# Kernel tuning notes

Hardware: AMD Instinct MI355X
Metric: run time of the kernel (lower is better)

Reference implementation:

```python
import jax, jax.numpy as jnp
import numpy as np
from jax import lax

B, CIN, H, W = 2, 512, 64, 64
NCLS = 5
CI = CIN // 4      # inter_channels = 128
CQ = CI // 8       # PAM query/key channels = 16
EPS = 1e-5


def setup_inputs() -> dict:
    key = jax.random.key(0)
    it = iter(jax.random.split(key, 48))

    def nrm(shape, s=0.05):
        return jax.random.normal(next(it), shape, jnp.float32) * s

    def bn(c):
        w = jax.random.uniform(next(it), (c,), jnp.float32, 0.5, 1.5)
        b = nrm((c,))
        m = nrm((c,))
        v = jax.random.uniform(next(it), (c,), jnp.float32, 0.5, 1.5)
        return w, b, m, v

    inp = {}
    inp['x'] = jax.random.normal(next(it), (B, CIN, H, W), jnp.float32)
    inp['bn_a_w'], inp['bn_a_b'], inp['bn_a_m'], inp['bn_a_v'] = bn(CIN)
    inp['conv_a_w'] = nrm((CI, CIN, 3, 3))
    inp['bn_c_w'], inp['bn_c_b'], inp['bn_c_m'], inp['bn_c_v'] = bn(CIN)
    inp['conv_c_w'] = nrm((CI, CIN, 3, 3))
    inp['pam_q_w'] = nrm((CQ, CI)); inp['pam_q_b'] = nrm((CQ,))
    inp['pam_k_w'] = nrm((CQ, CI)); inp['pam_k_b'] = nrm((CQ,))
    inp['pam_v_w'] = nrm((CI, CI)); inp['pam_v_b'] = nrm((CI,))
    inp['pam_gamma'] = nrm((1,), 0.5)
    inp['cam_gamma'] = nrm((1,), 0.5)
    inp['bn_a1_w'], inp['bn_a1_b'], inp['bn_a1_m'], inp['bn_a1_v'] = bn(CI)
    inp['conv_a1_w'] = nrm((CIN, CI)); inp['conv_a1_b'] = nrm((CIN,))
    inp['bn_c1_w'], inp['bn_c1_b'], inp['bn_c1_m'], inp['bn_c1_v'] = bn(CI)
    inp['conv_c1_w'] = nrm((CIN, CI)); inp['conv_c1_b'] = nrm((CIN,))
    inp['out_a_w'] = nrm((NCLS, CIN)); inp['out_a_b'] = nrm((NCLS,))
    inp['out_c_w'] = nrm((NCLS, CIN)); inp['out_c_b'] = nrm((NCLS,))
    inp['out_f_w'] = nrm((NCLS, CIN)); inp['out_f_b'] = nrm((NCLS,))
    return inp


def _bn_relu(x, w, b, m, v):
    # eval-mode BatchNorm2d followed by ReLU
    scale = (w / jnp.sqrt(v + EPS))[None, :, None, None]
    shift = (b - m * w / jnp.sqrt(v + EPS))[None, :, None, None]
    return jax.nn.relu(x * scale + shift)


def _conv3(x, w):
    return lax.conv_general_dilated(x, w, (1, 1), 'SAME',
                                    dimension_numbers=('NCHW', 'OIHW', 'NCHW'))


def _conv1(x, w, b):
    # 1x1 conv as channel matmul
    return jnp.einsum('oi,bihw->bohw', w, x) + b[None, :, None, None]


def _pam(x, wq, bq, wk, bk, wv, bv, gamma):
    Bc, C, Hh, Ww = x.shape
    N = Hh * Ww
    q = _conv1(x, wq, bq).reshape(Bc, -1, N)   # [B,CQ,N]
    k = _conv1(x, wk, bk).reshape(Bc, -1, N)   # [B,CQ,N]
    v = _conv1(x, wv, bv).reshape(Bc, C, N)    # [B,C,N]
    energy = jnp.einsum('bcn,bcm->bnm', q, k)  # [B,N,N]
    attn = jax.nn.softmax(energy, axis=-1)
    out = jnp.einsum('bcm,bnm->bcn', v, attn).reshape(Bc, C, Hh, Ww)
    return gamma * out + x


def _cam(x, gamma):
    Bc, C, Hh, Ww = x.shape
    N = Hh * Ww
    f = x.reshape(Bc, C, N)
    energy = jnp.einsum('bcn,bdn->bcd', f, f)                    # [B,C,C]
    energy_new = jnp.max(energy, -1, keepdims=True) - energy
    attn = jax.nn.softmax(energy_new, axis=-1)
    out = jnp.einsum('bcd,bdn->bcn', attn, f).reshape(Bc, C, Hh, Ww)
    return gamma * out + x


def reference(x, bn_a_w, bn_a_b, bn_a_m, bn_a_v, conv_a_w,
              bn_c_w, bn_c_b, bn_c_m, bn_c_v, conv_c_w,
              pam_q_w, pam_q_b, pam_k_w, pam_k_b, pam_v_w, pam_v_b,
              pam_gamma, cam_gamma,
              bn_a1_w, bn_a1_b, bn_a1_m, bn_a1_v, conv_a1_w, conv_a1_b,
              bn_c1_w, bn_c1_b, bn_c1_m, bn_c1_v, conv_c1_w, conv_c1_b,
              out_a_w, out_a_b, out_c_w, out_c_b, out_f_w, out_f_b):
    # position-attention branch
    sa = _conv3(_bn_relu(x, bn_a_w, bn_a_b, bn_a_m, bn_a_v), conv_a_w)
    sa = _pam(sa, pam_q_w, pam_q_b, pam_k_w, pam_k_b, pam_v_w, pam_v_b, pam_gamma)
    sa = _conv1(_bn_relu(sa, bn_a1_w, bn_a1_b, bn_a1_m, bn_a1_v), conv_a1_w, conv_a1_b)
    # channel-attention branch
    sc = _conv3(_bn_relu(x, bn_c_w, bn_c_b, bn_c_m, bn_c_v), conv_c_w)
    sc = _cam(sc, cam_gamma)
    sc = _conv1(_bn_relu(sc, bn_c1_w, bn_c1_b, bn_c1_m, bn_c1_v), conv_c1_w, conv_c1_b)
    feat_fusion = sa + sc
    # dropout is identity at eval time
    sa_out = _conv1(sa, out_a_w, out_a_b)
    sc_out = _conv1(sc, out_c_w, out_c_b)
    sasc_out = _conv1(feat_fusion, out_f_w, out_f_b)
    return (feat_fusion, sasc_out, sa_out, sc_out)
```

## Files before the change

kernel.cpp:

```cpp
#include <hip/hip_runtime.h>

using u16 = unsigned short;
using short8 = __attribute__((ext_vector_type(8))) short;
using f32x4 = __attribute__((ext_vector_type(4))) float;

struct alignas(8) U16x4 { u16 x, y, z, w; };

__device__ __forceinline__ float bf2f(u16 u) {
  return __uint_as_float(((unsigned int)u) << 16);
}
__device__ __forceinline__ u16 f2bf(float f) {
  unsigned int u = __float_as_uint(f);
  unsigned int r = u + 0x7FFFu + ((u >> 16) & 1u);
  return (u16)(r >> 16);
}

__global__ void k_prep_w(const float* __restrict__ wa, const float* __restrict__ wc,
                         u16* __restrict__ Wb) {
  int idx = blockIdx.x * 256 + threadIdx.x;
  int j = idx & 7;
  int l = (idx >> 3) & 63;
  int ks = (idx >> 9) & 3;
  int rest = idx >> 11;
  int tap = rest % 9;
  int rest2 = rest / 9;
  int chunk = rest2 & 3;
  int mt = (rest2 >> 2) & 7;
  int br = rest2 >> 5;
  int co = mt * 16 + (l & 15);
  int ci = chunk * 128 + ks * 32 + (l >> 4) * 8 + j;
  const float* w = br ? wc : wa;
  Wb[idx] = f2bf(w[co * 4608 + ci * 9 + tap]);
}

__global__ void k_prep_w1(const float* __restrict__ wa, const float* __restrict__ wc,
                          u16* __restrict__ W1b) {
  int idx = blockIdx.x * 256 + threadIdx.x;
  int j = idx & 7;
  int l = (idx >> 3) & 63;
  int ks = (idx >> 9) & 3;
  int cot = (idx >> 11) & 31;
  int br = idx >> 16;
  int co = cot * 16 + (l & 15);
  int ci = ks * 32 + (l >> 4) * 8 + j;
  const float* w = br ? wc : wa;
  W1b[idx] = f2bf(w[co * 128 + ci]);
}

__global__ void k_prep_wqkv(const float* __restrict__ wq, const float* __restrict__ wk,
                            const float* __restrict__ wv, u16* __restrict__ Wq) {
  int idx = blockIdx.x * 256 + threadIdx.x;
  if (idx >= 20480) return;
  int j = idx & 7;
  int l = (idx >> 3) & 63;
  int ks = (idx >> 9) & 3;
  int cot = idx >> 11;
  int co = cot * 16 + (l & 15);
  int ci = ks * 32 + (l >> 4) * 8 + j;
  float w = co < 16 ? wq[co * 128 + ci]
          : (co < 32 ? wk[(co - 16) * 128 + ci] : wv[(co - 32) * 128 + ci]);
  Wq[idx] = f2bf(w);
}

__global__ __launch_bounds__(256) void k_bnrelu2t(const float* __restrict__ x,
    const float* __restrict__ wa, const float* __restrict__ ba,
    const float* __restrict__ ma, const float* __restrict__ va,
    const float* __restrict__ wc, const float* __restrict__ bc,
    const float* __restrict__ mc, const float* __restrict__ vc,
    u16* __restrict__ xa16, u16* __restrict__ xcb16) {
  __shared__ float sA[512], bA[512], sC[512], bC[512];
  __shared__ u16 ta[64 * 136], tc[64 * 136];
  int t = threadIdx.x;
  int h = blockIdx.x, b = blockIdx.y;
  for (int c = t; c < 512; c += 256) {
    float s1 = wa[c] * rsqrtf(va[c] + 1e-5f);
    sA[c] = s1; bA[c] = ba[c] - ma[c] * s1;
    float s2 = wc[c] * rsqrtf(vc[c] + 1e-5f);
    sC[c] = s2; bC[c] = bc[c] - mc[c] * s2;
  }
  __syncthreads();
  const float* xb = x + ((size_t)b << 21) + (h << 6);
  u16* oa = xa16 + ((size_t)b << 21) + ((size_t)h << 15);
  u16* oc = xcb16 + ((size_t)b << 21) + ((size_t)h << 15);
  int w = t & 63, cg = t >> 6;
  for (int c0 = 0; c0 < 512; c0 += 128) {
#pragma unroll
    for (int i = 0; i < 8; ++i) {
      int cl = cg * 4 + i * 16;
      int c = c0 + cl;
      const float* xp = xb + (size_t)c * 4096 + w;
      float v0 = xp[0], v1 = xp[4096], v2 = xp[8192], v3 = xp[12288];
      U16x4 pa, pc;
      pa.x = f2bf(fmaxf(fmaf(v0, sA[c], bA[c]), 0.f));
      pa.y = f2bf(fmaxf(fmaf(v1, sA[c + 1], bA[c + 1]), 0.f));
      pa.z = f2bf(fmaxf(fmaf(v2, sA[c + 2], bA[c + 2]), 0.f));
      pa.w = f2bf(fmaxf(fmaf(v3, sA[c + 3], bA[c + 3]), 0.f));
      pc.x = f2bf(fmaxf(fmaf(v0, sC[c], bC[c]), 0.f));
      pc.y = f2bf(fmaxf(fmaf(v1, sC[c + 1], bC[c + 1]), 0.f));
      pc.z = f2bf(fmaxf(fmaf(v2, sC[c + 2], bC[c + 2]), 0.f));
      pc.w = f2bf(fmaxf(fmaf(v3, sC[c + 3], bC[c + 3]), 0.f));
      *(U16x4*)(ta + w * 136 + cl) = pa;
      *(U16x4*)(tc + w * 136 + cl) = pc;
    }
    __syncthreads();
#pragma unroll
    for (int i = 0; i < 4; ++i) {
      int idx = t + i * 256;
      int ww = idx >> 4, c8 = (idx & 15) << 3;
      *(short8*)(oa + (size_t)ww * 512 + c0 + c8) = *(const short8*)(ta + ww * 136 + c8);
      *(short8*)(oc + (size_t)ww * 512 + c0 + c8) = *(const short8*)(tc + ww * 136 + c8);
    }
    __syncthreads();
  }
}

__global__ __launch_bounds__(256) void k_conv3n(
    const u16* __restrict__ xa16, const u16* __restrict__ xcb16,
    const u16* __restrict__ Wb,
    float* __restrict__ sa0, float* __restrict__ sc0,
    u16* __restrict__ sa_nhwc, u16* __restrict__ sc16h, u16* __restrict__ sc16l) {
  __shared__ u16 xs[3 * 66 * 136];
  int t = threadIdx.x;
  int h = blockIdx.x;
  int z = blockIdx.y; int b = z & 1, br = z >> 1;
  const u16* xb = (br ? xcb16 : xa16) + ((size_t)b << 21);
  const u16* wb = Wb + (size_t)br * 589824;
  float* out = (br ? sc0 : sa0) + (((size_t)b * 128) << 12) + (h << 6);

  int lane = t & 63, wave = t >> 6;
  int mi = lane & 15, quad = lane >> 4;

  if (t < 96) {
    int dh = t >> 5, side = (t >> 4) & 1, c8 = t & 15;
    short8 z8 = {0, 0, 0, 0, 0, 0, 0, 0};
    *(short8*)(xs + (dh * 66 + side * 65) * 136 + c8 * 8) = z8;
  }

  f32x4 acc[2][4] = {};

  const u16* wlane = wb + lane * 8;
  const u16* bbase0 = xs + mi * 136 + quad * 8;

  for (int chunk = 0; chunk < 4; ++chunk) {
    int ci0 = chunk << 7;
    __syncthreads();
#pragma unroll
    for (int dh = 0; dh < 3; ++dh) {
      int hh = h + dh - 1;
      bool val = (hh >= 0) && (hh < 64);
      const u16* src = xb + (((size_t)hh << 6) << 9) + ci0;
#pragma unroll
      for (int i = 0; i < 4; ++i) {
        int idx = t + i * 256;
        int w = idx >> 4, c8 = (idx & 15) << 3;
        short8 v = {0, 0, 0, 0, 0, 0, 0, 0};
        if (val) v = *(const short8*)(src + ((size_t)w << 9) + c8);
        *(short8*)(xs + (dh * 66 + 1 + w) * 136 + c8) = v;
      }
    }
    __syncthreads();
    const u16* wchunk = wlane + (size_t)(wave * 2 * 4 + chunk) * 36 * 512;
#pragma unroll
    for (int tap = 0; tap < 9; ++tap) {
      const int dh = tap / 3, dw = tap % 3;
      const u16* bp = bbase0 + (dh * 66 + dw) * 136;
      const u16* wt0 = wchunk + tap * 2048;
      const u16* wt1 = wt0 + 73728;
#pragma unroll
      for (int ks = 0; ks < 4; ++ks) {
        short8 a0 = *(const short8*)(wt0 + ks * 512);
        short8 a1 = *(const short8*)(wt1 + ks * 512);
#pragma unroll
        for (int nt = 0; nt < 4; ++nt) {
          short8 bf = *(const short8*)(bp + nt * 2176 + ks * 32);
          acc[0][nt] = __builtin_amdgcn_mfma_f32_16x16x32_bf16(a0, bf, acc[0][nt], 0, 0, 0);
          acc[1][nt] = __builtin_amdgcn_mfma_f32_16x16x32_bf16(a1, bf, acc[1][nt], 0, 0, 0);
        }
      }
    }
  }
#pragma unroll
  for (int m = 0; m < 2; ++m)
#pragma unroll
    for (int nt = 0; nt < 4; ++nt)
#pragma unroll
      for (int r = 0; r < 4; ++r) {
        int co = wave * 32 + m * 16 + quad * 4 + r;
        out[((size_t)co << 12) + nt * 16 + mi] = acc[m][nt][r];
      }
  if (br == 0) {
    u16* dstq = sa_nhwc + ((size_t)b << 19) + ((size_t)h << 6) * 128;
#pragma unroll
    for (int m = 0; m < 2; ++m)
#pragma unroll
      for (int nt = 0; nt < 4; ++nt) {
        U16x4 v4;
        v4.x = f2bf(acc[m][nt][0]); v4.y = f2bf(acc[m][nt][1]);
        v4.z = f2bf(acc[m][nt][2]); v4.w = f2bf(acc[m][nt][3]);
        *(U16x4*)(dstq + (size_t)(nt * 16 + mi) * 128 + wave * 32 + m * 16 + quad * 4) = v4;
      }
  } else {
    u16* dh_ = sc16h + ((size_t)b << 19) + (h << 6);
    u16* dl_ = sc16l + ((size_t)b << 19) + (h << 6);
#pragma unroll
    for (int m = 0; m < 2; ++m)
#pragma unroll
      for (int nt = 0; nt < 4; ++nt)
#pragma unroll
        for (int r = 0; r < 4; ++r) {
          int co = wave * 32 + m * 16 + quad * 4 + r;
          float xv = acc[m][nt][r];
          u16 hi = f2bf(xv);
          float lo = xv - bf2f(hi);
          size_t o = ((size_t)co << 12) + nt * 16 + mi;
          dh_[o] = hi;
          dl_[o] = f2bf(lo);
        }
  }
}

__global__ __launch_bounds__(256) void k_qkv(
    const u16* __restrict__ sa_nhwc, const u16* __restrict__ Wqkvb,
    const float* __restrict__ bq, const float* __restrict__ bk,
    const float* __restrict__ bv,
    float* __restrict__ qb, float* __restrict__ kbuf, u16* __restrict__ vt16) {
  __shared__ float bs[160];
  int t = threadIdx.x;
  int b = blockIdx.y, n0 = blockIdx.x * 128;
  if (t < 160) bs[t] = t < 16 ? bq[t] : (t < 32 ? bk[t - 16] : bv[t - 32]);
  __syncthreads();
  int lane = t & 63, wave = t >> 6;
  int mi = lane & 15, quad = lane >> 4;
  const u16* xb = sa_nhwc + ((size_t)b << 19) + (size_t)n0 * 128;
  const u16* wb = Wqkvb + lane * 8;
  f32x4 acc[2][10] = {};
  short8 bf[2][4];
#pragma unroll
  for (int ns = 0; ns < 2; ++ns) {
    int n = wave * 32 + ns * 16 + mi;
#pragma unroll
    for (int ks = 0; ks < 4; ++ks)
      bf[ns][ks] = *(const short8*)(xb + (size_t)n * 128 + ks * 32 + quad * 8);
  }
#pragma unroll
  for (int cot = 0; cot < 10; ++cot) {
    short8 a0 = *(const short8*)(wb + (size_t)(cot * 4 + 0) * 512);
    short8 a1 = *(const short8*)(wb + (size_t)(cot * 4 + 1) * 512);
    short8 a2 = *(const short8*)(wb + (size_t)(cot * 4 + 2) * 512);
    short8 a3 = *(const short8*)(wb + (size_t)(cot * 4 + 3) * 512);
#pragma unroll
    for (int ns = 0; ns < 2; ++ns) {
      acc[ns][cot] = __builtin_amdgcn_mfma_f32_16x16x32_bf16(a0, bf[ns][0], acc[ns][cot], 0, 0, 0);
      acc[ns][cot] = __builtin_amdgcn_mfma_f32_16x16x32_bf16(a1, bf[ns][1], acc[ns][cot], 0, 0, 0);
      acc[ns][cot] = __builtin_amdgcn_mfma_f32_16x16x32_bf16(a2, bf[ns][2], acc[ns][cot], 0, 0, 0);
      acc[ns][cot] = __builtin_amdgcn_mfma_f32_16x16x32_bf16(a3, bf[ns][3], acc[ns][cot], 0, 0, 0);
    }
  }
#pragma unroll
  for (int cot = 0; cot < 10; ++cot)
#pragma unroll
    for (int ns = 0; ns < 2; ++ns)
#pragma unroll
      for (int r = 0; r < 4; ++r) {
        int co = cot * 16 + quad * 4 + r;
        int n = n0 + wave * 32 + ns * 16 + mi;
        float v = acc[ns][cot][r] + bs[co];
        if (co < 16) qb[((b * 16 + co) << 12) + n] = v;
        else if (co < 32) kbuf[((b * 16 + co - 16) << 12) + n] = v;
        else vt16[((size_t)(b * 128 + co - 32) << 12) + n] = f2bf(v);
      }
}

__global__ __launch_bounds__(256) void k_pam_stats(const float* __restrict__ qb,
    const float* __restrict__ kb, float* __restrict__ rmax, float* __restrict__ rinv) {
  int t = threadIdx.x, lane = t & 63, wid = t >> 6;
  int b = blockIdx.y;
  int n0 = blockIdx.x * 16 + wid * 4;
  float qreg[4][16];
  const float* qp = qb + ((size_t)b * 16 << 12) + n0;
#pragma unroll
  for (int ch = 0; ch < 16; ++ch)
#pragma unroll
    for (int j = 0; j < 4; ++j) qreg[j][ch] = qp[(ch << 12) + j];
  const float* kp = kb + ((size_t)b * 16 << 12);
  float mx[4], se[4];
#pragma unroll
  for (int j = 0; j < 4; ++j) { mx[j] = -1e30f; se[j] = 0.f; }
  for (int m4 = lane * 4; m4 < 4096; m4 += 256) {
    float e[4][4] = {};
#pragma unroll
    for (int ch = 0; ch < 16; ++ch) {
      float4 kv = *(const float4*)(kp + (ch << 12) + m4);
#pragma unroll
      for (int j = 0; j < 4; ++j) {
        float qv = qreg[j][ch];
        e[j][0] = fmaf(qv, kv.x, e[j][0]);
        e[j][1] = fmaf(qv, kv.y, e[j][1]);
        e[j][2] = fmaf(qv, kv.z, e[j][2]);
        e[j][3] = fmaf(qv, kv.w, e[j][3]);
      }
    }
#pragma unroll
    for (int j = 0; j < 4; ++j) {
      float lm = fmaxf(fmaxf(e[j][0], e[j][1]), fmaxf(e[j][2], e[j][3]));
      float nm = fmaxf(mx[j], lm);
      se[j] = se[j] * __expf(mx[j] - nm)
            + __expf(e[j][0] - nm) + __expf(e[j][1] - nm)
            + __expf(e[j][2] - nm) + __expf(e[j][3] - nm);
      mx[j] = nm;
    }
  }
#pragma unroll
  for (int off = 32; off >= 1; off >>= 1) {
#pragma unroll
    for (int j = 0; j < 4; ++j) {
      float om = __shfl_xor(mx[j], off);
      float os = __shfl_xor(se[j], off);
      float nm = fmaxf(mx[j], om);
      se[j] = se[j] * __expf(mx[j] - nm) + os * __expf(om - nm);
      mx[j] = nm;
    }
  }
  if (lane == 0) {
#pragma unroll
    for (int j = 0; j < 4; ++j) {
      rmax[(b << 12) + n0 + j] = mx[j];
      rinv[(b << 12) + n0 + j] = 1.f / se[j];
    }
  }
}

__global__ __launch_bounds__(512, 4) void k_pam_pv(const float* __restrict__ qb,
    const float* __restrict__ kb, const u16* __restrict__ vt16,
    const float* __restrict__ rmax, const float* __restrict__ rinv,
    const float* __restrict__ gamma, float* __restrict__ pvpart) {
  constexpr int PSTR = 264;
  __shared__ float ks[2][16 * 256];
  __shared__ u16 pL[32 * PSTR];
  int t = threadIdx.x;
  int b = blockIdx.y, n0 = blockIdx.x * 32;
  int mbeg = blockIdx.z << 11;
  int lane = t & 63, wave = t >> 6;
  int nl = t & 31, mg = t >> 5;
  int mi = lane & 15, quad = lane >> 4;
  int c0 = wave * 16;
  float qreg[16];
  const float* qp = qb + ((size_t)b * 16 << 12) + n0 + nl;
#pragma unroll
  for (int ch = 0; ch < 16; ++ch) qreg[ch] = qp[ch << 12];
  float mv = rmax[(b << 12) + n0 + nl];
  float iv = rinv[(b << 12) + n0 + nl];
  const float* kpb = kb + ((size_t)b * 16 << 12) + mbeg;
  const u16* vb = vt16 + ((size_t)b * 128 << 12);
  f32x4 acc[2] = {};
#pragma unroll
  for (int k = 0; k < 8; ++k) {
    int idx = t + k * 512;
    ks[0][idx] = kpb[((idx >> 8) << 12) + (idx & 255)];
  }
  __syncthreads();
  int cur = 0;
  for (int it = 0; it < 8; ++it) {
    int m0 = mbeg + (it << 8);
    short8 vreg[8];
#pragma unroll
    for (int ksl = 0; ksl < 8; ++ksl)
      vreg[ksl] = *(const short8*)(vb + ((size_t)(c0 + mi) << 12) + m0 + ksl * 32 + quad * 8);
    float kreg[8];
    if (it < 7) {
#pragma unroll
      for (int k = 0; k < 8; ++k) {
        int idx = t + k * 512;
        kreg[k] = kpb[((idx >> 8) << 12) + ((it + 1) << 8) + (idx & 255)];
      }
    }
    float e[16] = {};
    const float* kbase = &ks[cur][mg << 4];
#pragma unroll
    for (int ch = 0; ch < 16; ++ch) {
      float qv = qreg[ch];
      const float* kp2 = kbase + (ch << 8);
      float4 kv0 = *(const float4*)(kp2);
      float4 kv1 = *(const float4*)(kp2 + 4);
      float4 kv2 = *(const float4*)(kp2 + 8);
      float4 kv3 = *(const float4*)(kp2 + 12);
      e[0] = fmaf(qv, kv0.x, e[0]);  e[1] = fmaf(qv, kv0.y, e[1]);
      e[2] = fmaf(qv, kv0.z, e[2]);  e[3] = fmaf(qv, kv0.w, e[3]);
      e[4] = fmaf(qv, kv1.x, e[4]);  e[5] = fmaf(qv, kv1.y, e[5]);
      e[6] = fmaf(qv, kv1.z, e[6]);  e[7] = fmaf(qv, kv1.w, e[7]);
      e[8] = fmaf(qv, kv2.x, e[8]);  e[9] = fmaf(qv, kv2.y, e[9]);
      e[10] = fmaf(qv, kv2.z, e[10]); e[11] = fmaf(qv, kv2.w, e[11]);
      e[12] = fmaf(qv, kv3.x, e[12]); e[13] = fmaf(qv, kv3.y, e[13]);
      e[14] = fmaf(qv, kv3.z, e[14]); e[15] = fmaf(qv, kv3.w, e[15]);
    }
    short8 p0, p1;
#pragma unroll
    for (int j = 0; j < 8; ++j) {
      p0[j] = (short)f2bf(__expf(fminf(e[j] - mv, 0.f)) * iv);
      p1[j] = (short)f2bf(__expf(fminf(e[j + 8] - mv, 0.f)) * iv);
    }
    {
      u16* pw = pL + nl * PSTR + (mg << 4);
      *(short8*)(pw) = p0;
      *(short8*)(pw + 8) = p1;
    }
    __syncthreads();
    if (it < 7) {
#pragma unroll
      for (int k = 0; k < 8; ++k) {
        int idx = t + k * 512;
        ks[cur ^ 1][idx] = kreg[k];
      }
    }
#pragma unroll
    for (int ksl = 0; ksl < 8; ++ksl) {
      const u16* pb0 = pL + mi * PSTR + ksl * 32 + quad * 8;
      short8 b0 = *(const short8*)(pb0);
      short8 b1 = *(const short8*)(pb0 + 16 * PSTR);
      acc[0] = __builtin_amdgcn_mfma_f32_16x16x32_bf16(vreg[ksl], b0, acc[0], 0, 0, 0);
      acc[1] = __builtin_amdgcn_mfma_f32_16x16x32_bf16(vreg[ksl], b1, acc[1], 0, 0, 0);
    }
    __syncthreads();
    cur ^= 1;
  }
  float g = gamma[0];
  float* dst = pvpart + (((size_t)(blockIdx.z * 2 + b) * 128) << 12);
#pragma unroll
  for (int nh = 0; nh < 2; ++nh)
#pragma unroll
    for (int r = 0; r < 4; ++r) {
      int c = c0 + quad * 4 + r;
      dst[((size_t)c << 12) + n0 + nh * 16 + mi] = g * acc[nh][r];
    }
}

__global__ __launch_bounds__(512) void k_cam_energy_m(
    const u16* __restrict__ sc16h, const u16* __restrict__ sc16l,
    float* __restrict__ epart) {
  int t = threadIdx.x;
  int ti = blockIdx.x, kc = blockIdx.y, b = blockIdx.z;
  int lane = t & 63, wave = t >> 6;
  int mi = lane & 15, quad = lane >> 4;
  const u16* fh = sc16h + ((size_t)b << 19);
  const u16* fl = sc16l + ((size_t)b << 19);
  size_t ao = ((size_t)(ti * 16 + mi) << 12) + (kc << 9) + quad * 8;
  size_t bo = ((size_t)(wave * 16 + mi) << 12) + (kc << 9) + quad * 8;
  const u16* ah = fh + ao; const u16* al = fl + ao;
  const u16* bh = fh + bo; const u16* bl = fl + bo;
  f32x4 acc = {};
#pragma unroll
  for (int k = 0; k < 16; ++k) {
    short8 vah = *(const short8*)(ah + k * 32);
    short8 val = *(const short8*)(al + k * 32);
    short8 vbh = *(const short8*)(bh + k * 32);
    short8 vbl = *(const short8*)(bl + k * 32);
    acc = __builtin_amdgcn_mfma_f32_16x16x32_bf16(vah, vbh, acc, 0, 0, 0);
    acc = __builtin_amdgcn_mfma_f32_16x16x32_bf16(vah, vbl, acc, 0, 0, 0);
    acc = __builtin_amdgcn_mfma_f32_16x16x32_bf16(val, vbh, acc, 0, 0, 0);
  }
  float* ep = epart + (((size_t)(kc * 2 + b)) << 14);
#pragma unroll
  for (int r = 0; r < 4; ++r)
    ep[((ti * 16 + quad * 4 + r) << 7) + wave * 16 + mi] = acc[r];
}

__global__ void k_cam_softmax(const float* __restrict__ epart, float* __restrict__ attn) {
  int lane = threadIdx.x;
  int c = blockIdx.x, b = blockIdx.y;
  float e0 = 0.f, e1 = 0.f;
#pragma unroll
  for (int kc = 0; kc < 8; ++kc) {
    const float* ep = epart + (((size_t)(kc * 2 + b)) << 14) + (c << 7);
    e0 += ep[lane];
    e1 += ep[lane + 64];
  }
  float mn = fminf(e0, e1);
#pragma unroll
  for (int off = 32; off >= 1; off >>= 1) mn = fminf(mn, __shfl_xor(mn, off));
  float p0 = __expf(fminf(mn - e0, 0.f)), p1 = __expf(fminf(mn - e1, 0.f));
  float s = p0 + p1;
#pragma unroll
  for (int off = 32; off >= 1; off >>= 1) s += __shfl_xor(s, off);
  float inv = 1.f / s;
  float* a = attn + ((b * 128 + c) << 7);
  a[lane] = p0 * inv;
  a[lane + 64] = p1 * inv;
}

__global__ __launch_bounds__(256) void k_cam_out(const float* __restrict__ f,
    const float* __restrict__ attn, const float* __restrict__ gamma,
    float* __restrict__ sc1) {
  __shared__ float at2[128 * 16];
  int t = threadIdx.x;
  int b = blockIdx.z, c0 = blockIdx.y * 16;
  int n = blockIdx.x * 256 + t;
  for (int idx = t; idx < 2048; idx += 256) {
    int d = idx >> 4, cc = idx & 15;
    at2[idx] = attn[((b * 128 + c0 + cc) << 7) + d];
  }
  __syncthreads();
  float acc[16] = {};
  const float* fb = f + ((size_t)b * 128 << 12) + n;
  for (int d = 0; d < 128; ++d) {
    float fv = fb[d << 12];
    const float* ap = at2 + d * 16;
#pragma unroll
    for (int cc = 0; cc < 16; ++cc) acc[cc] = fmaf(ap[cc], fv, acc[cc]);
  }
  float g = gamma[0];
#pragma unroll
  for (int cc = 0; cc < 16; ++cc) {
    size_t o = ((size_t)(b * 128 + c0 + cc) << 12) + n;
    sc1[o] = fmaf(g, acc[cc], f[o]);
  }
}

__global__ __launch_bounds__(256, 2) void k_bout_m(
    const float* __restrict__ sa0, const float* __restrict__ pvpart,
    const float* __restrict__ sc1,
    const float* __restrict__ wa_, const float* __restrict__ ba_,
    const float* __restrict__ ma_, const float* __restrict__ va_,
    const float* __restrict__ wc_, const float* __restrict__ bc_,
    const float* __restrict__ mc_, const float* __restrict__ vc_,
    const u16* __restrict__ W1b, const float* __restrict__ Ba,
    const float* __restrict__ Bc,
    u16* __restrict__ sa2, u16* __restrict__ sc2) {
  __shared__ u16 xl[32 * 136];
  __shared__ float scl[128], shf[128];
  int t = threadIdx.x;
  int n0 = blockIdx.x * 32;
  int b = blockIdx.y, br = blockIdx.z;
  const float* bw = br ? wc_ : wa_;
  const float* bb = br ? bc_ : ba_;
  const float* bm = br ? mc_ : ma_;
  const float* bvv = br ? vc_ : va_;
  if (t < 128) {
    float s = bw[t] * rsqrtf(bvv[t] + 1e-5f);
    scl[t] = s;
    shf[t] = bb[t] - bm[t] * s;
  }
  __syncthreads();
  {
    int nl = t & 31, cio = t >> 5;
    const float* s0 = (br ? sc1 : sa0) + ((size_t)b * 128 << 12) + n0 + nl;
    const float* p0 = pvpart + ((size_t)b * 128 << 12) + n0 + nl;
    const float* p1 = pvpart + (((size_t)(2 + b) * 128) << 12) + n0 + nl;
#pragma unroll
    for (int half = 0; half < 2; ++half) {
      short8 v;
#pragma unroll
      for (int i = 0; i < 8; ++i) {
        int ci = cio * 16 + half * 8 + i;
        float xv = s0[(size_t)ci << 12];
        if (!br) xv += p0[(size_t)ci << 12] + p1[(size_t)ci << 12];
        v[i] = (short)f2bf(fmaxf(fmaf(xv, scl[ci], shf[ci]), 0.f));
      }
      *(short8*)(xl + nl * 136 + cio * 16 + half * 8) = v;
    }
  }
  __syncthreads();
  int lane = t & 63, wave = t >> 6;
  int mi = lane & 15, quad = lane >> 4;
  const u16* wb = W1b + (size_t)br * 65536 + lane * 8;
  f32x4 acc[8][2] = {};
#pragma unroll
  for (int ks = 0; ks < 4; ++ks) {
    short8 b0 = *(const short8*)(xl + mi * 136 + ks * 32 + quad * 8);
    short8 b1 = *(const short8*)(xl + (16 + mi) * 136 + ks * 32 + quad * 8);
#pragma unroll
    for (int ct = 0; ct < 8; ++ct) {
      int cot = wave * 8 + ct;
      short8 a = *(const short8*)(wb + ((size_t)(cot * 4 + ks) << 9));
      acc[ct][0] = __builtin_amdgcn_mfma_f32_16x16x32_bf16(a, b0, acc[ct][0], 0, 0, 0);
      acc[ct][1] = __builtin_amdgcn_mfma_f32_16x16x32_bf16(a, b1, acc[ct][1], 0, 0, 0);
    }
  }
  const float* Bs = br ? Bc : Ba;
  u16* dst = br ? sc2 : sa2;
#pragma unroll
  for (int ct = 0; ct < 8; ++ct)
#pragma unroll
    for (int nh = 0; nh < 2; ++nh)
#pragma unroll
      for (int r = 0; r < 4; ++r) {
        int co = (wave * 8 + ct) * 16 + quad * 4 + r;
        dst[((size_t)(b * 512 + co) << 12) + n0 + nh * 16 + mi] =
            f2bf(acc[ct][nh][r] + Bs[co]);
      }
}

__global__ __launch_bounds__(256) void k_heads(const u16* __restrict__ sa2,
    const u16* __restrict__ sc2,
    const float* __restrict__ wf, const float* __restrict__ wa, const float* __restrict__ wc,
    float* __restrict__ outFusion, float* __restrict__ clsacc) {
  __shared__ float lw[3 * 5 * 64];
  int t = threadIdx.x;
  int b = blockIdx.y, co0 = blockIdx.z * 64;
  int n = blockIdx.x * 256 + t;
  for (int idx = t; idx < 960; idx += 256) {
    int arr = idx / 320, rest = idx - arr * 320;
    int cls = rest >> 6, cc = rest & 63;
    const float* w = arr == 0 ? wf : (arr == 1 ? wa : wc);
    lw[idx] = w[cls * 512 + co0 + cc];
  }
  __syncthreads();
  float af[5] = {}, aa[5] = {}, ac[5] = {};
  for (int cc = 0; cc < 64; ++cc) {
    size_t o = ((size_t)(b * 512 + co0 + cc) << 12) + n;
    float a = bf2f(sa2[o]), c = bf2f(sc2[o]);
    float s = a + c;
    outFusion[o] = s;
#pragma unroll
    for (int cls = 0; cls < 5; ++cls) {
      af[cls] = fmaf(lw[0 * 320 + cls * 64 + cc], s, af[cls]);
      aa[cls] = fmaf(lw[1 * 320 + cls * 64 + cc], a, aa[cls]);
      ac[cls] = fmaf(lw[2 * 320 + cls * 64 + cc], c, ac[cls]);
    }
  }
#pragma unroll
  for (int cls = 0; cls < 5; ++cls) {
    int o = ((b * 5 + cls) << 12) + n;
    atomicAdd(&clsacc[o], af[cls]);
    atomicAdd(&clsacc[40960 + o], aa[cls]);
    atomicAdd(&clsacc[81920 + o], ac[cls]);
  }
}

__global__ void k_heads_final(const float* __restrict__ clsacc,
    const float* __restrict__ bf_, const float* __restrict__ ba_,
    const float* __restrict__ bc_, float* __restrict__ outCls) {
  int idx = blockIdx.x * 256 + threadIdx.x;
  int arr = idx / 40960;
  int rest = idx - arr * 40960;
  int cls = (rest >> 12) % 5;
  const float* bp = arr == 0 ? bf_ : (arr == 1 ? ba_ : bc_);
  outCls[idx] = clsacc[idx] + bp[cls];
}

extern "C" void kernel_launch(void* const* d_in, const int* in_sizes, int n_in,
                              void* d_out, int out_size, void* d_ws, size_t ws_size,
                              hipStream_t stream) {
  (void)in_sizes; (void)n_in; (void)out_size; (void)ws_size;
  const float* x      = (const float*)d_in[0];
  const float* bnaw   = (const float*)d_in[1];
  const float* bnab   = (const float*)d_in[2];
  const float* bnam   = (const float*)d_in[3];
  const float* bnav   = (const float*)d_in[4];
  const float* convaw = (const float*)d_in[5];
  const float* bncw   = (const float*)d_in[6];
  const float* bncb   = (const float*)d_in[7];
  const float* bncm   = (const float*)d_in[8];
  const float* bncv   = (const float*)d_in[9];
  const float* convcw = (const float*)d_in[10];
  const float* pqw    = (const float*)d_in[11];
  const float* pqb    = (const float*)d_in[12];
  const float* pkw    = (const float*)d_in[13];
  const float* pkb    = (const float*)d_in[14];
  const float* pvw    = (const float*)d_in[15];
  const float* pvb    = (const float*)d_in[16];
  const float* pgam   = (const float*)d_in[17];
  const float* cgam   = (const float*)d_in[18];
  const float* bna1w  = (const float*)d_in[19];
  const float* bna1b  = (const float*)d_in[20];
  const float* bna1m  = (const float*)d_in[21];
  const float* bna1v  = (const float*)d_in[22];
  const float* conva1w = (const float*)d_in[23];
  const float* conva1b = (const float*)d_in[24];
  const float* bnc1w  = (const float*)d_in[25];
  const float* bnc1b  = (const float*)d_in[26];
  const float* bnc1m  = (const float*)d_in[27];
  const float* bnc1v  = (const float*)d_in[28];
  const float* convc1w = (const float*)d_in[29];
  const float* convc1b = (const float*)d_in[30];
  const float* outaw  = (const float*)d_in[31];
  const float* outab  = (const float*)d_in[32];
  const float* outcw  = (const float*)d_in[33];
  const float* outcb  = (const float*)d_in[34];
  const float* outfw  = (const float*)d_in[35];
  const float* outfb  = (const float*)d_in[36];

  char* wsb = (char*)d_ws;
  size_t off = 0;
  auto take = [&](size_t bytes) -> void* {
    void* p = wsb + off;
    off += (bytes + 255) & ~(size_t)255;
    return p;
  };
  u16*   Wb    = (u16*)take((size_t)2 * 128 * 9 * 512 * 2);
  u16*   W1b   = (u16*)take((size_t)2 * 512 * 128 * 2);
  u16*   Wqkvb = (u16*)take((size_t)160 * 128 * 2);
  u16*   xa16  = (u16*)take((size_t)2 * 512 * 4096 * 2);
  u16*   xcb16 = (u16*)take((size_t)2 * 512 * 4096 * 2);
  float* sa0   = (float*)take((size_t)2 * 128 * 4096 * 4);
  float* sc0   = (float*)take((size_t)2 * 128 * 4096 * 4);
  u16*   sa_nhwc = (u16*)take((size_t)2 * 4096 * 128 * 2);
  u16*   sc16h = (u16*)take((size_t)2 * 128 * 4096 * 2);
  u16*   sc16l = (u16*)take((size_t)2 * 128 * 4096 * 2);
  float* qb    = (float*)take((size_t)2 * 16 * 4096 * 4);
  float* kbuf  = (float*)take((size_t)2 * 16 * 4096 * 4);
  u16*   vt16  = (u16*)take((size_t)2 * 128 * 4096 * 2);
  float* rmax  = (float*)take((size_t)2 * 4096 * 4);
  float* rinv  = (float*)take((size_t)2 * 4096 * 4);
  float* pvpart = (float*)take((size_t)2 * 2 * 128 * 4096 * 4);
  float* sc1   = (float*)take((size_t)2 * 128 * 4096 * 4);
  float* epart = (float*)take((size_t)8 * 2 * 128 * 128 * 4);
  float* attn  = (float*)take((size_t)2 * 128 * 128 * 4);
  u16*   sa2   = (u16*)take((size_t)2 * 512 * 4096 * 2);
  u16*   sc2   = (u16*)take((size_t)2 * 512 * 4096 * 2);
  float* clsacc = (float*)take((size_t)3 * 2 * 5 * 4096 * 4);

  float* outF = (float*)d_out;
  float* outCls = outF + (size_t)2 * 512 * 4096;

  hipMemsetAsync(clsacc, 0, (size_t)3 * 2 * 5 * 4096 * 4, stream);

  k_prep_w<<<4608, 256, 0, stream>>>(convaw, convcw, Wb);
  k_prep_w1<<<512, 256, 0, stream>>>(conva1w, convc1w, W1b);
  k_prep_wqkv<<<80, 256, 0, stream>>>(pqw, pkw, pvw, Wqkvb);
  k_bnrelu2t<<<dim3(64, 2), 256, 0, stream>>>(x, bnaw, bnab, bnam, bnav,
                                              bncw, bncb, bncm, bncv, xa16, xcb16);
  k_conv3n<<<dim3(64, 4), 256, 0, stream>>>(xa16, xcb16, Wb, sa0, sc0,
                                            sa_nhwc, sc16h, sc16l);
  k_qkv<<<dim3(32, 2), 256, 0, stream>>>(sa_nhwc, Wqkvb, pqb, pkb, pvb,
                                         qb, kbuf, vt16);
  k_pam_stats<<<dim3(256, 2), 256, 0, stream>>>(qb, kbuf, rmax, rinv);
  k_pam_pv<<<dim3(128, 2, 2), 512, 0, stream>>>(qb, kbuf, vt16, rmax, rinv, pgam, pvpart);
  k_cam_energy_m<<<dim3(8, 8, 2), 512, 0, stream>>>(sc16h, sc16l, epart);
  k_cam_softmax<<<dim3(128, 2), 64, 0, stream>>>(epart, attn);
  k_cam_out<<<dim3(16, 8, 2), 256, 0, stream>>>(sc0, attn, cgam, sc1);
  k_bout_m<<<dim3(128, 2, 2), 256, 0, stream>>>(sa0, pvpart, sc1,
      bna1w, bna1b, bna1m, bna1v, bnc1w, bnc1b, bnc1m, bnc1v,
      W1b, conva1b, convc1b, sa2, sc2);
  k_heads<<<dim3(16, 2, 8), 256, 0, stream>>>(sa2, sc2, outfw, outaw, outcw, outF, clsacc);
  k_heads_final<<<480, 256, 0, stream>>>(clsacc, outfb, outab, outcb, outCls);
}
```

Baseline: 349.8 us.

## Split conv3 output channels across two blocks and double-buffer weight fragments

The 3x3 conv kernel now launches twice as many blocks, each computing half the output channels (one 16-channel M tile per wave instead of two). The weight fragments for the next tap are loaded into registers while the current tap's MFMAs run, and launch_bounds asks for two blocks per CU. The aim is to fill more CUs (256 blocks was fewer than the GPU's CU count) and hide global weight-load latency. In exchange, each input tile is staged into LDS twice, and each B fragment read from LDS now feeds only one MFMA instead of two.

```diff
diff --git a/kernel.cpp b/kernel.cpp
--- a/kernel.cpp
+++ b/kernel.cpp
@@ -114,7 +114,7 @@
   }
 }
 
-__global__ __launch_bounds__(256) void k_conv3n(
+__global__ __launch_bounds__(256, 2) void k_conv3n(
     const u16* __restrict__ xa16, const u16* __restrict__ xcb16,
     const u16* __restrict__ Wb,
     float* __restrict__ sa0, float* __restrict__ sc0,
@@ -123,12 +123,14 @@
   int t = threadIdx.x;
   int h = blockIdx.x;
   int z = blockIdx.y; int b = z & 1, br = z >> 1;
+  int cosplit = blockIdx.z;
   const u16* xb = (br ? xcb16 : xa16) + ((size_t)b << 21);
   const u16* wb = Wb + (size_t)br * 589824;
   float* out = (br ? sc0 : sa0) + (((size_t)b * 128) << 12) + (h << 6);
 
   int lane = t & 63, wave = t >> 6;
   int mi = lane & 15, quad = lane >> 4;
+  int mt = cosplit * 4 + wave;
 
   if (t < 96) {
     int dh = t >> 5, side = (t >> 4) & 1, c8 = t & 15;
@@ -136,7 +138,7 @@
     *(short8*)(xs + (dh * 66 + side * 65) * 136 + c8 * 8) = z8;
   }
 
-  f32x4 acc[2][4] = {};
+  f32x4 acc[4] = {};
 
   const u16* wlane = wb + lane * 8;
   const u16* bbase0 = xs + mi * 136 + quad * 8;
@@ -159,63 +161,64 @@
       }
     }
     __syncthreads();
-    const u16* wchunk = wlane + (size_t)(wave * 2 * 4 + chunk) * 36 * 512;
+    const u16* wchunk = wlane + (size_t)(mt * 4 + chunk) * 18432;
+    short8 wreg[2][4];
+#pragma unroll
+    for (int ks = 0; ks < 4; ++ks)
+      wreg[0][ks] = *(const short8*)(wchunk + ks * 512);
 #pragma unroll
     for (int tap = 0; tap < 9; ++tap) {
+      const int cb = tap & 1;
+      if (tap < 8) {
+        const u16* wn = wchunk + (tap + 1) * 2048;
+#pragma unroll
+        for (int ks = 0; ks < 4; ++ks)
+          wreg[cb ^ 1][ks] = *(const short8*)(wn + ks * 512);
+      }
       const int dh = tap / 3, dw = tap % 3;
       const u16* bp = bbase0 + (dh * 66 + dw) * 136;
-      const u16* wt0 = wchunk + tap * 2048;
-      const u16* wt1 = wt0 + 73728;
 #pragma unroll
       for (int ks = 0; ks < 4; ++ks) {
-        short8 a0 = *(const short8*)(wt0 + ks * 512);
-        short8 a1 = *(const short8*)(wt1 + ks * 512);
+        short8 a = wreg[cb][ks];
 #pragma unroll
         for (int nt = 0; nt < 4; ++nt) {
           short8 bf = *(const short8*)(bp + nt * 2176 + ks * 32);
-          acc[0][nt] = __builtin_amdgcn_mfma_f32_16x16x32_bf16(a0, bf, acc[0][nt], 0, 0, 0);
-          acc[1][nt] = __builtin_amdgcn_mfma_f32_16x16x32_bf16(a1, bf, acc[1][nt], 0, 0, 0);
+          acc[nt] = __builtin_amdgcn_mfma_f32_16x16x32_bf16(a, bf, acc[nt], 0, 0, 0);
         }
       }
     }
   }
 #pragma unroll
-  for (int m = 0; m < 2; ++m)
-#pragma unroll
-    for (int nt = 0; nt < 4; ++nt)
-#pragma unroll
-      for (int r = 0; r < 4; ++r) {
-        int co = wave * 32 + m * 16 + quad * 4 + r;
-        out[((size_t)co << 12) + nt * 16 + mi] = acc[m][nt][r];
-      }
+  for (int nt = 0; nt < 4; ++nt)
+#pragma unroll
+    for (int r = 0; r < 4; ++r) {
+      int co = mt * 16 + quad * 4 + r;
+      out[((size_t)co << 12) + nt * 16 + mi] = acc[nt][r];
+    }
   if (br == 0) {
     u16* dstq = sa_nhwc + ((size_t)b << 19) + ((size_t)h << 6) * 128;
 #pragma unroll
-    for (int m = 0; m < 2; ++m)
-#pragma unroll
-      for (int nt = 0; nt < 4; ++nt) {
-        U16x4 v4;
-        v4.x = f2bf(acc[m][nt][0]); v4.y = f2bf(acc[m][nt][1]);
-        v4.z = f2bf(acc[m][nt][2]); v4.w = f2bf(acc[m][nt][3]);
-        *(U16x4*)(dstq + (size_t)(nt * 16 + mi) * 128 + wave * 32 + m * 16 + quad * 4) = v4;
-      }
+    for (int nt = 0; nt < 4; ++nt) {
+      U16x4 v4;
+      v4.x = f2bf(acc[nt][0]); v4.y = f2bf(acc[nt][1]);
+      v4.z = f2bf(acc[nt][2]); v4.w = f2bf(acc[nt][3]);
+      *(U16x4*)(dstq + (size_t)(nt * 16 + mi) * 128 + mt * 16 + quad * 4) = v4;
+    }
   } else {
     u16* dh_ = sc16h + ((size_t)b << 19) + (h << 6);
     u16* dl_ = sc16l + ((size_t)b << 19) + (h << 6);
 #pragma unroll
-    for (int m = 0; m < 2; ++m)
-#pragma unroll
-      for (int nt = 0; nt < 4; ++nt)
-#pragma unroll
-        for (int r = 0; r < 4; ++r) {
-          int co = wave * 32 + m * 16 + quad * 4 + r;
-          float xv = acc[m][nt][r];
-          u16 hi = f2bf(xv);
-          float lo = xv - bf2f(hi);
-          size_t o = ((size_t)co << 12) + nt * 16 + mi;
-          dh_[o] = hi;
-          dl_[o] = f2bf(lo);
-        }
+    for (int nt = 0; nt < 4; ++nt)
+#pragma unroll
+      for (int r = 0; r < 4; ++r) {
+        int co = mt * 16 + quad * 4 + r;
+        float xv = acc[nt][r];
+        u16 hi = f2bf(xv);
+        float lo = xv - bf2f(hi);
+        size_t o = ((size_t)co << 12) + nt * 16 + mi;
+        dh_[o] = hi;
+        dl_[o] = f2bf(lo);
+      }
   }
 }
 
@@ -719,8 +722,8 @@
   k_prep_wqkv<<<80, 256, 0, stream>>>(pqw, pkw, pvw, Wqkvb);
   k_bnrelu2t<<<dim3(64, 2), 256, 0, stream>>>(x, bnaw, bnab, bnam, bnav,
                                               bncw, bncb, bncm, bncv, xa16, xcb16);
-  k_conv3n<<<dim3(64, 4), 256, 0, stream>>>(xa16, xcb16, Wb, sa0, sc0,
-                                            sa_nhwc, sc16h, sc16l);
+  k_conv3n<<<dim3(64, 4, 2), 256, 0, stream>>>(xa16, xcb16, Wb, sa0, sc0,
+                                               sa_nhwc, sc16h, sc16l);
   k_qkv<<<dim3(32, 2), 256, 0, stream>>>(sa_nhwc, Wqkvb, pqb, pkb, pvb,
                                          qb, kbuf, vt16);
   k_pam_stats<<<dim3(256, 2), 256, 0, stream>>>(qb, kbuf, rmax, rinv);
```

After: 347.1 us. Within noise of the previous version (-0.8%).
